# Optimization experiments

Hardware: AMD Instinct MI355X
Metric: run time of the kernel (lower is better)

Reference implementation:

```python
import jax, jax.numpy as jnp
import numpy as np

B, S, D, I = 4, 2048, 4096, 11008

def setup_inputs() -> dict:
    key = jax.random.key(0)
    ks = jax.random.split(key, 7)
    x = jax.random.normal(ks[0], (B, S, D), dtype=jnp.float32)
    # int8 weights stored as int32 carriers with int8-range values
    gate_w = jax.random.randint(ks[1], (I, D), -127, 128, dtype=jnp.int32)
    up_w = jax.random.randint(ks[2], (I, D), -127, 128, dtype=jnp.int32)
    down_w = jax.random.randint(ks[3], (D, I), -127, 128, dtype=jnp.int32)
    # per-tensor scales (fp16 in original; fp32 here for a clean baseline)
    gate_s = jax.random.uniform(ks[4], (1,), dtype=jnp.float32) * 0.01 + 0.001
    up_s = jax.random.uniform(ks[5], (1,), dtype=jnp.float32) * 0.01 + 0.001
    down_s = jax.random.uniform(ks[6], (1,), dtype=jnp.float32) * 0.01 + 0.001
    return {"x": x, "gate_w": gate_w, "gate_s": gate_s,
            "up_w": up_w, "up_s": up_s, "down_w": down_w, "down_s": down_s}

def _dequant_matmul(x, w_int8, scale):
    # y = x @ (w * s)^T == (x @ w^T) * s  (per-tensor scale commutes)
    w = w_int8.astype(x.dtype)
    return jnp.einsum('bsd,od->bso', x, w) * scale

def reference(x, gate_w, gate_s, up_w, up_s, down_w, down_s):
    gate = jax.nn.silu(_dequant_matmul(x, gate_w, gate_s))  # [B,S,I]
    up = _dequant_matmul(x, up_w, up_s)                      # [B,S,I]
    out = _dequant_matmul(gate * up, down_w, down_s)         # [B,S,D]
    return out.astype(x.dtype)
```

## Files before the change

### kernel.cpp

```cpp
#include <hip/hip_runtime.h>
#include <hip/hip_fp16.h>

#define MTOK 8192
#define DDIM 4096
#define IDIM 11008

#define BM 128
#define BN 128
#define BK 64

typedef _Float16 f16x4 __attribute__((ext_vector_type(4)));
typedef _Float16 f16x8 __attribute__((ext_vector_type(8)));
typedef float    f32x4 __attribute__((ext_vector_type(4)));

__global__ __launch_bounds__(256) void cvt_x_kernel(const float* __restrict__ src,
                                                    _Float16* __restrict__ dst, int n4) {
  int stride = gridDim.x * blockDim.x;
  for (int i = blockIdx.x * blockDim.x + threadIdx.x; i < n4; i += stride) {
    float4 v = ((const float4*)src)[i];
    f16x4 h;
    h.x = (_Float16)v.x; h.y = (_Float16)v.y; h.z = (_Float16)v.z; h.w = (_Float16)v.w;
    ((f16x4*)dst)[i] = h;
  }
}

__global__ __launch_bounds__(256) void cvt_w_kernel(const int* __restrict__ src,
                                                    _Float16* __restrict__ dst, int n4) {
  int stride = gridDim.x * blockDim.x;
  for (int i = blockIdx.x * blockDim.x + threadIdx.x; i < n4; i += stride) {
    int4 v = ((const int4*)src)[i];
    f16x4 h;
    h.x = (_Float16)v.x; h.y = (_Float16)v.y; h.z = (_Float16)v.z; h.w = (_Float16)v.w;
    ((f16x4*)dst)[i] = h;
  }
}

__device__ __forceinline__ void stage_tile(const _Float16* __restrict__ gbase, int ldk,
                                           _Float16* stile, int tid) {
#pragma unroll
  for (int it = 0; it < 4; ++it) {
    int slot = it * 256 + tid;
    int r = slot >> 3, c = slot & 7;
    int csrc = c ^ (r & 7);
    const _Float16* gp = gbase + (long)r * ldk + csrc * 8;
    __builtin_amdgcn_global_load_lds(
        (const __attribute__((address_space(1))) void*)gp,
        (__attribute__((address_space(3))) void*)(stile + slot * 8),
        16, 0, 0);
  }
}

__device__ __forceinline__ f16x8 frag_ld(const _Float16* s, int row, int cbase) {
  int c = cbase ^ (row & 7);
  return *(const f16x8*)(s + (row * 8 + c) * 8);
}

__global__ __launch_bounds__(256, 2) void gemm_gateup(
    const _Float16* __restrict__ X, const _Float16* __restrict__ Wg,
    const _Float16* __restrict__ Wu, const float* __restrict__ gs_p,
    const float* __restrict__ us_p, _Float16* __restrict__ H) {
  __shared__ _Float16 sA[BM * BK] __attribute__((aligned(16)));
  __shared__ _Float16 sG[BN * BK] __attribute__((aligned(16)));
  __shared__ _Float16 sU[BN * BK] __attribute__((aligned(16)));

  int tid = threadIdx.x;
  int bm = blockIdx.x, bn = blockIdx.y;
  int lane = tid & 63, w = tid >> 6;
  int wr = (w >> 1) * 64, wc = (w & 1) * 64;
  int lr = lane & 15, q = lane >> 4;

  const _Float16* Abase = X + (long)bm * BM * DDIM;
  const _Float16* Gbase = Wg + (long)bn * BN * DDIM;
  const _Float16* Ubase = Wu + (long)bn * BN * DDIM;

  f32x4 accg[4][4], accu[4][4];
#pragma unroll
  for (int i = 0; i < 4; ++i)
#pragma unroll
    for (int j = 0; j < 4; ++j) {
      accg[i][j] = (f32x4){0.f, 0.f, 0.f, 0.f};
      accu[i][j] = (f32x4){0.f, 0.f, 0.f, 0.f};
    }

  for (int k0 = 0; k0 < DDIM; k0 += BK) {
    stage_tile(Abase + k0, DDIM, sA, tid);
    stage_tile(Gbase + k0, DDIM, sG, tid);
    stage_tile(Ubase + k0, DDIM, sU, tid);
    __syncthreads();
#pragma unroll
    for (int kk = 0; kk < 2; ++kk) {
      int cbase = kk * 4 + q;
      f16x8 a[4], bg[4], bu[4];
#pragma unroll
      for (int i = 0; i < 4; ++i) a[i] = frag_ld(sA, wr + i * 16 + lr, cbase);
#pragma unroll
      for (int j = 0; j < 4; ++j) {
        bg[j] = frag_ld(sG, wc + j * 16 + lr, cbase);
        bu[j] = frag_ld(sU, wc + j * 16 + lr, cbase);
      }
#pragma unroll
      for (int i = 0; i < 4; ++i)
#pragma unroll
        for (int j = 0; j < 4; ++j) {
          accg[i][j] = __builtin_amdgcn_mfma_f32_16x16x32_f16(a[i], bg[j], accg[i][j], 0, 0, 0);
          accu[i][j] = __builtin_amdgcn_mfma_f32_16x16x32_f16(a[i], bu[j], accu[i][j], 0, 0, 0);
        }
    }
    __syncthreads();
  }

  float gs = gs_p[0], us = us_p[0];
#pragma unroll
  for (int i = 0; i < 4; ++i)
#pragma unroll
    for (int j = 0; j < 4; ++j)
#pragma unroll
      for (int r = 0; r < 4; ++r) {
        long m = (long)bm * BM + wr + i * 16 + q * 4 + r;
        long n = (long)bn * BN + wc + j * 16 + lr;
        float g = accg[i][j][r] * gs;
        float u = accu[i][j][r] * us;
        float sg = g / (1.0f + __expf(-g));
        H[m * IDIM + n] = (_Float16)(sg * u * 0.00390625f);
      }
}

__global__ __launch_bounds__(256, 2) void gemm_down(
    const _Float16* __restrict__ Hin, const _Float16* __restrict__ Wd,
    const float* __restrict__ ds_p, float* __restrict__ Out) {
  __shared__ _Float16 sA[BM * BK] __attribute__((aligned(16)));
  __shared__ _Float16 sB0[BN * BK] __attribute__((aligned(16)));
  __shared__ _Float16 sB1[BN * BK] __attribute__((aligned(16)));

  int tid = threadIdx.x;
  int bm = blockIdx.x, bn = blockIdx.y;
  int lane = tid & 63, w = tid >> 6;
  int wr = (w >> 1) * 64, wc = (w & 1) * 64;
  int lr = lane & 15, q = lane >> 4;

  const _Float16* Abase = Hin + (long)bm * BM * IDIM;
  const _Float16* B0base = Wd + (long)(bn * 256) * IDIM;
  const _Float16* B1base = Wd + (long)(bn * 256 + 128) * IDIM;

  f32x4 acc0[4][4], acc1[4][4];
#pragma unroll
  for (int i = 0; i < 4; ++i)
#pragma unroll
    for (int j = 0; j < 4; ++j) {
      acc0[i][j] = (f32x4){0.f, 0.f, 0.f, 0.f};
      acc1[i][j] = (f32x4){0.f, 0.f, 0.f, 0.f};
    }

  for (int k0 = 0; k0 < IDIM; k0 += BK) {
    stage_tile(Abase + k0, IDIM, sA, tid);
    stage_tile(B0base + k0, IDIM, sB0, tid);
    stage_tile(B1base + k0, IDIM, sB1, tid);
    __syncthreads();
#pragma unroll
    for (int kk = 0; kk < 2; ++kk) {
      int cbase = kk * 4 + q;
      f16x8 a[4], b0[4], b1[4];
#pragma unroll
      for (int i = 0; i < 4; ++i) a[i] = frag_ld(sA, wr + i * 16 + lr, cbase);
#pragma unroll
      for (int j = 0; j < 4; ++j) {
        b0[j] = frag_ld(sB0, wc + j * 16 + lr, cbase);
        b1[j] = frag_ld(sB1, wc + j * 16 + lr, cbase);
      }
#pragma unroll
      for (int i = 0; i < 4; ++i)
#pragma unroll
        for (int j = 0; j < 4; ++j) {
          acc0[i][j] = __builtin_amdgcn_mfma_f32_16x16x32_f16(a[i], b0[j], acc0[i][j], 0, 0, 0);
          acc1[i][j] = __builtin_amdgcn_mfma_f32_16x16x32_f16(a[i], b1[j], acc1[i][j], 0, 0, 0);
        }
    }
    __syncthreads();
  }

  float scale = ds_p[0] * 256.0f;
#pragma unroll
  for (int i = 0; i < 4; ++i)
#pragma unroll
    for (int j = 0; j < 4; ++j)
#pragma unroll
      for (int r = 0; r < 4; ++r) {
        long m = (long)bm * BM + wr + i * 16 + q * 4 + r;
        long n = (long)bn * 256 + wc + j * 16 + lr;
        Out[m * DDIM + n] = acc0[i][j][r] * scale;
        Out[m * DDIM + n + 128] = acc1[i][j][r] * scale;
      }
}

extern "C" void kernel_launch(void* const* d_in, const int* in_sizes, int n_in,
                              void* d_out, int out_size, void* d_ws, size_t ws_size,
                              hipStream_t stream) {
  const float* x  = (const float*)d_in[0];
  const int*   gw = (const int*)d_in[1];
  const float* gs = (const float*)d_in[2];
  const int*   uw = (const int*)d_in[3];
  const float* us = (const float*)d_in[4];
  const int*   dw = (const int*)d_in[5];
  const float* ds = (const float*)d_in[6];
  float* out = (float*)d_out;

  char* ws = (char*)d_ws;
  _Float16* xf  = (_Float16*)(ws);
  _Float16* gwf = (_Float16*)(ws + 67108864L);
  _Float16* uwf = (_Float16*)(ws + 157286400L);
  _Float16* dwf = (_Float16*)(ws + 247463936L);
  _Float16* h   = (_Float16*)(ws + 337641472L);

  cvt_x_kernel<<<2048, 256, 0, stream>>>(x, xf, (MTOK * DDIM) / 4);
  cvt_w_kernel<<<2048, 256, 0, stream>>>(gw, gwf, (IDIM * DDIM) / 4);
  cvt_w_kernel<<<2048, 256, 0, stream>>>(uw, uwf, (IDIM * DDIM) / 4);
  cvt_w_kernel<<<2048, 256, 0, stream>>>(dw, dwf, (DDIM * IDIM) / 4);

  dim3 g1(MTOK / BM, IDIM / BN);
  gemm_gateup<<<g1, 256, 0, stream>>>(xf, gwf, uwf, gs, us, h);

  dim3 g2(MTOK / BM, DDIM / 256);
  gemm_down<<<g2, 256, 0, stream>>>(h, dwf, ds, out);
}
```

Measured before the change: 2.574 ms.

## Double-buffer LDS tiles and enlarge block tile to 256 rows with 512 threads

Both GEMM kernels now use 8-wave (512-thread) blocks covering a 256x128 output tile. The operand tiles for step k+1 are staged into a second LDS buffer while step k is computed, replacing the load-sync-compute-sync loop with one waitcnt and barrier per iteration. The goal is to overlap global-to-LDS transfers with MFMA work and to reuse the activation tile across more output rows per weight load. In exchange, each block now uses about 128KB of LDS, which limits a CU to one resident block. The launch-bounds occupancy hint may also squeeze the VGPR budget for the 128-float accumulator set per wave, risking register spills.

```diff
diff --git a/kernel.cpp b/kernel.cpp
--- a/kernel.cpp
+++ b/kernel.cpp
@@ -5,9 +5,10 @@
 #define DDIM 4096
 #define IDIM 11008
 
-#define BM 128
+#define BM 256
 #define BN 128
 #define BK 64
+#define NTHR 512
 
 typedef _Float16 f16x4 __attribute__((ext_vector_type(4)));
 typedef _Float16 f16x8 __attribute__((ext_vector_type(8)));
@@ -35,11 +36,12 @@
   }
 }
 
+template<int ROWS>
 __device__ __forceinline__ void stage_tile(const _Float16* __restrict__ gbase, int ldk,
                                            _Float16* stile, int tid) {
 #pragma unroll
-  for (int it = 0; it < 4; ++it) {
-    int slot = it * 256 + tid;
+  for (int it = 0; it < (ROWS * 8) / NTHR; ++it) {
+    int slot = it * NTHR + tid;
     int r = slot >> 3, c = slot & 7;
     int csrc = c ^ (r & 7);
     const _Float16* gp = gbase + (long)r * ldk + csrc * 8;
@@ -55,18 +57,19 @@
   return *(const f16x8*)(s + (row * 8 + c) * 8);
 }
 
-__global__ __launch_bounds__(256, 2) void gemm_gateup(
+__global__ __launch_bounds__(NTHR, 2) void gemm_gateup(
     const _Float16* __restrict__ X, const _Float16* __restrict__ Wg,
     const _Float16* __restrict__ Wu, const float* __restrict__ gs_p,
     const float* __restrict__ us_p, _Float16* __restrict__ H) {
-  __shared__ _Float16 sA[BM * BK] __attribute__((aligned(16)));
-  __shared__ _Float16 sG[BN * BK] __attribute__((aligned(16)));
-  __shared__ _Float16 sU[BN * BK] __attribute__((aligned(16)));
+  constexpr int ASZ = BM * BK;
+  constexpr int BSZ = BN * BK;
+  constexpr int BUF = ASZ + 2 * BSZ;
+  __shared__ _Float16 lds[2 * BUF] __attribute__((aligned(16)));
 
   int tid = threadIdx.x;
   int bm = blockIdx.x, bn = blockIdx.y;
   int lane = tid & 63, w = tid >> 6;
-  int wr = (w >> 1) * 64, wc = (w & 1) * 64;
+  int wm = (w >> 1) * 64, wn = (w & 1) * 64;
   int lr = lane & 15, q = lane >> 4;
 
   const _Float16* Abase = X + (long)bm * BM * DDIM;
@@ -82,21 +85,33 @@
       accu[i][j] = (f32x4){0.f, 0.f, 0.f, 0.f};
     }
 
-  for (int k0 = 0; k0 < DDIM; k0 += BK) {
-    stage_tile(Abase + k0, DDIM, sA, tid);
-    stage_tile(Gbase + k0, DDIM, sG, tid);
-    stage_tile(Ubase + k0, DDIM, sU, tid);
-    __syncthreads();
+  stage_tile<BM>(Abase, DDIM, lds, tid);
+  stage_tile<BN>(Gbase, DDIM, lds + ASZ, tid);
+  stage_tile<BN>(Ubase, DDIM, lds + ASZ + BSZ, tid);
+  asm volatile("s_waitcnt vmcnt(0)" ::: "memory");
+  __builtin_amdgcn_s_barrier();
+
+  constexpr int NT = DDIM / BK;
+#pragma unroll 1
+  for (int t = 0; t < NT; ++t) {
+    _Float16* cb = lds + (t & 1) * BUF;
+    if (t + 1 < NT) {
+      _Float16* nb = lds + ((t + 1) & 1) * BUF;
+      int k0 = (t + 1) * BK;
+      stage_tile<BM>(Abase + k0, DDIM, nb, tid);
+      stage_tile<BN>(Gbase + k0, DDIM, nb + ASZ, tid);
+      stage_tile<BN>(Ubase + k0, DDIM, nb + ASZ + BSZ, tid);
+    }
 #pragma unroll
     for (int kk = 0; kk < 2; ++kk) {
       int cbase = kk * 4 + q;
       f16x8 a[4], bg[4], bu[4];
 #pragma unroll
-      for (int i = 0; i < 4; ++i) a[i] = frag_ld(sA, wr + i * 16 + lr, cbase);
+      for (int i = 0; i < 4; ++i) a[i] = frag_ld(cb, wm + i * 16 + lr, cbase);
 #pragma unroll
       for (int j = 0; j < 4; ++j) {
-        bg[j] = frag_ld(sG, wc + j * 16 + lr, cbase);
-        bu[j] = frag_ld(sU, wc + j * 16 + lr, cbase);
+        bg[j] = frag_ld(cb + ASZ, wn + j * 16 + lr, cbase);
+        bu[j] = frag_ld(cb + ASZ + BSZ, wn + j * 16 + lr, cbase);
       }
 #pragma unroll
       for (int i = 0; i < 4; ++i)
@@ -106,7 +121,8 @@
           accu[i][j] = __builtin_amdgcn_mfma_f32_16x16x32_f16(a[i], bu[j], accu[i][j], 0, 0, 0);
         }
     }
-    __syncthreads();
+    asm volatile("s_waitcnt vmcnt(0)" ::: "memory");
+    __builtin_amdgcn_s_barrier();
   }
 
   float gs = gs_p[0], us = us_p[0];
@@ -116,8 +132,8 @@
     for (int j = 0; j < 4; ++j)
 #pragma unroll
       for (int r = 0; r < 4; ++r) {
-        long m = (long)bm * BM + wr + i * 16 + q * 4 + r;
-        long n = (long)bn * BN + wc + j * 16 + lr;
+        long m = (long)bm * BM + wm + i * 16 + q * 4 + r;
+        long n = (long)bn * BN + wn + j * 16 + lr;
         float g = accg[i][j][r] * gs;
         float u = accu[i][j][r] * us;
         float sg = g / (1.0f + __expf(-g));
@@ -125,20 +141,21 @@
       }
 }
 
-__global__ __launch_bounds__(256, 2) void gemm_down(
+__global__ __launch_bounds__(NTHR, 2) void gemm_down(
     const _Float16* __restrict__ Hin, const _Float16* __restrict__ Wd,
     const float* __restrict__ ds_p, float* __restrict__ Out) {
-  __shared__ _Float16 sA[BM * BK] __attribute__((aligned(16)));
-  __shared__ _Float16 sB0[BN * BK] __attribute__((aligned(16)));
-  __shared__ _Float16 sB1[BN * BK] __attribute__((aligned(16)));
+  constexpr int ASZ = BM * BK;
+  constexpr int BSZ = BN * BK;
+  constexpr int BUF = ASZ + 2 * BSZ;
+  __shared__ _Float16 lds[2 * BUF] __attribute__((aligned(16)));
 
   int tid = threadIdx.x;
   int bm = blockIdx.x, bn = blockIdx.y;
   int lane = tid & 63, w = tid >> 6;
-  int wr = (w >> 1) * 64, wc = (w & 1) * 64;
+  int wm = (w >> 1) * 64, wn = (w & 1) * 64;
   int lr = lane & 15, q = lane >> 4;
 
-  const _Float16* Abase = Hin + (long)bm * BM * IDIM;
+  const _Float16* Abase  = Hin + (long)bm * BM * IDIM;
   const _Float16* B0base = Wd + (long)(bn * 256) * IDIM;
   const _Float16* B1base = Wd + (long)(bn * 256 + 128) * IDIM;
 
@@ -151,21 +168,33 @@
       acc1[i][j] = (f32x4){0.f, 0.f, 0.f, 0.f};
     }
 
-  for (int k0 = 0; k0 < IDIM; k0 += BK) {
-    stage_tile(Abase + k0, IDIM, sA, tid);
-    stage_tile(B0base + k0, IDIM, sB0, tid);
-    stage_tile(B1base + k0, IDIM, sB1, tid);
-    __syncthreads();
+  stage_tile<BM>(Abase, IDIM, lds, tid);
+  stage_tile<BN>(B0base, IDIM, lds + ASZ, tid);
+  stage_tile<BN>(B1base, IDIM, lds + ASZ + BSZ, tid);
+  asm volatile("s_waitcnt vmcnt(0)" ::: "memory");
+  __builtin_amdgcn_s_barrier();
+
+  constexpr int NT = IDIM / BK;
+#pragma unroll 1
+  for (int t = 0; t < NT; ++t) {
+    _Float16* cb = lds + (t & 1) * BUF;
+    if (t + 1 < NT) {
+      _Float16* nb = lds + ((t + 1) & 1) * BUF;
+      int k0 = (t + 1) * BK;
+      stage_tile<BM>(Abase + k0, IDIM, nb, tid);
+      stage_tile<BN>(B0base + k0, IDIM, nb + ASZ, tid);
+      stage_tile<BN>(B1base + k0, IDIM, nb + ASZ + BSZ, tid);
+    }
 #pragma unroll
     for (int kk = 0; kk < 2; ++kk) {
       int cbase = kk * 4 + q;
       f16x8 a[4], b0[4], b1[4];
 #pragma unroll
-      for (int i = 0; i < 4; ++i) a[i] = frag_ld(sA, wr + i * 16 + lr, cbase);
+      for (int i = 0; i < 4; ++i) a[i] = frag_ld(cb, wm + i * 16 + lr, cbase);
 #pragma unroll
       for (int j = 0; j < 4; ++j) {
-        b0[j] = frag_ld(sB0, wc + j * 16 + lr, cbase);
-        b1[j] = frag_ld(sB1, wc + j * 16 + lr, cbase);
+        b0[j] = frag_ld(cb + ASZ, wn + j * 16 + lr, cbase);
+        b1[j] = frag_ld(cb + ASZ + BSZ, wn + j * 16 + lr, cbase);
       }
 #pragma unroll
       for (int i = 0; i < 4; ++i)
@@ -175,7 +204,8 @@
           acc1[i][j] = __builtin_amdgcn_mfma_f32_16x16x32_f16(a[i], b1[j], acc1[i][j], 0, 0, 0);
         }
     }
-    __syncthreads();
+    asm volatile("s_waitcnt vmcnt(0)" ::: "memory");
+    __builtin_amdgcn_s_barrier();
   }
 
   float scale = ds_p[0] * 256.0f;
@@ -185,8 +215,8 @@
     for (int j = 0; j < 4; ++j)
 #pragma unroll
       for (int r = 0; r < 4; ++r) {
-        long m = (long)bm * BM + wr + i * 16 + q * 4 + r;
-        long n = (long)bn * 256 + wc + j * 16 + lr;
+        long m = (long)bm * BM + wm + i * 16 + q * 4 + r;
+        long n = (long)bn * 256 + wn + j * 16 + lr;
         Out[m * DDIM + n] = acc0[i][j][r] * scale;
         Out[m * DDIM + n + 128] = acc1[i][j][r] * scale;
       }
@@ -217,8 +247,8 @@
   cvt_w_kernel<<<2048, 256, 0, stream>>>(dw, dwf, (DDIM * IDIM) / 4);
 
   dim3 g1(MTOK / BM, IDIM / BN);
-  gemm_gateup<<<g1, 256, 0, stream>>>(xf, gwf, uwf, gs, us, h);
+  gemm_gateup<<<g1, NTHR, 0, stream>>>(xf, gwf, uwf, gs, us, h);
 
   dim3 g2(MTOK / BM, DDIM / 256);
-  gemm_down<<<g2, 256, 0, stream>>>(h, dwf, ds, out);
-}
+  gemm_down<<<g2, NTHR, 0, stream>>>(h, dwf, ds, out);
+}
```

After: 2.386 ms. -7.3%, faster.
